# Performance work log

Measured on AMD Instinct MI355X. Metric: run time of the kernel, lower is better.

The kernel has to match this reference:

```python
import jax, jax.numpy as jnp
import numpy as np

MARGIN = 2.0
EPS = 1e-6  # F.pairwise_distance default: norm of (x1 - x2 + eps)

N, D = 4096, 768


def setup_inputs() -> dict:
    key = jax.random.key(0)
    k1, k2, k3 = jax.random.split(key, 3)
    image_embedding = jax.random.normal(k1, (N, D), dtype=jnp.float32)
    text_embedding = jax.random.normal(k2, (N, D), dtype=jnp.float32)
    ground_truth = jax.random.randint(k3, (N, N), 0, 2, dtype=jnp.int32)
    return {
        "image_embedding": image_embedding,
        "text_embedding": text_embedding,
        "ground_truth": ground_truth,
    }


def reference(image_embedding, text_embedding, ground_truth):
    d = image_embedding.shape[1]
    # Pairwise squared distance with pairwise_distance's +eps on the diff:
    # ||a - b + eps||^2 = ||a||^2 + ||b||^2 - 2 a.b + 2 eps (sum a - sum b) + d eps^2
    sa = jnp.sum(image_embedding * image_embedding, axis=1)   # [n]
    sb = jnp.sum(text_embedding * text_embedding, axis=1)     # [n]
    dot = image_embedding @ text_embedding.T                  # [n, n]
    ra = jnp.sum(image_embedding, axis=1)                     # [n]
    rb = jnp.sum(text_embedding, axis=1)                      # [n]
    sq = (sa[:, None] + sb[None, :] - 2.0 * dot
          + 2.0 * EPS * (ra[:, None] - rb[None, :]) + d * EPS * EPS)
    dist = jnp.sqrt(jnp.maximum(sq, 0.0))                     # [n, n]
    label = ground_truth.astype(dist.dtype)
    hinge = jnp.maximum(MARGIN - dist, 0.0)
    loss = jnp.mean((1.0 - label) * dist * dist + label * hinge * hinge)
    return loss
```

## Files before the change

kernel.cpp:

```cpp
#include <hip/hip_runtime.h>
#include <hip/hip_bf16.h>
#include <stdint.h>
#include <stddef.h>


#define NROWS 4096
#define DIM   768
#define BM    128
#define BN    128
#define BK    32
#define MARGIN 2.0f
#define EPSV   1e-6f

typedef __bf16 bf16_t;
typedef bf16_t bf16x8 __attribute__((ext_vector_type(8)));
typedef float  f32x4  __attribute__((ext_vector_type(4)));

__global__ __launch_bounds__(256) void prep_kernel(
    const float* __restrict__ A, const float* __restrict__ B,
    bf16_t* __restrict__ Ab, bf16_t* __restrict__ Bb,
    float* __restrict__ sa, float* __restrict__ sb,
    float* __restrict__ ra, float* __restrict__ rb)
{
    const int row  = blockIdx.x;
    const int isB  = blockIdx.y;
    const float* X = isB ? B : A;
    bf16_t* Xb     = isB ? Bb : Ab;
    float* sdst    = isB ? sb : sa;
    float* rdst    = isB ? rb : ra;

    const int t = threadIdx.x;
    const float* xr = X + (size_t)row * DIM;
    float v0 = xr[t], v1 = xr[t + 256], v2 = xr[t + 512];
    bf16_t* xb = Xb + (size_t)row * DIM;
    xb[t]       = (bf16_t)v0;
    xb[t + 256] = (bf16_t)v1;
    xb[t + 512] = (bf16_t)v2;

    float sum = v0 + v1 + v2;
    float sq  = v0 * v0 + v1 * v1 + v2 * v2;
    #pragma unroll
    for (int off = 32; off > 0; off >>= 1) {
        sum += __shfl_down(sum, off);
        sq  += __shfl_down(sq,  off);
    }
    __shared__ float red[8];
    const int wave = t >> 6;
    if ((t & 63) == 0) { red[wave] = sum; red[4 + wave] = sq; }
    __syncthreads();
    if (t == 0) {
        rdst[row] = (red[0] + red[1]) + (red[2] + red[3]);
        sdst[row] = (red[4] + red[5]) + (red[6] + red[7]);
    }
}

__global__ __launch_bounds__(256) void loss_kernel(
    const bf16_t* __restrict__ A, const bf16_t* __restrict__ B,
    const float* __restrict__ sa, const float* __restrict__ sb,
    const float* __restrict__ ra, const float* __restrict__ rb,
    const int* __restrict__ gt, float* __restrict__ out)
{
    __shared__ __align__(16) bf16_t As[BM * BK];
    __shared__ __align__(16) bf16_t Bs[BN * BK];
    __shared__ float redp[4];

    const int tid  = threadIdx.x;
    const int wave = tid >> 6;
    const int lane = tid & 63;
    const int m0 = blockIdx.y * BM;
    const int n0 = blockIdx.x * BN;

    f32x4 acc[4][4] = {};

    const int lrow   = lane >> 2;
    const int kchunk = (lane & 3) ^ (lrow & 3);

    const int fr = lane & 15;
    const int q  = lane >> 4;
    const int wm = (wave >> 1) * 64;
    const int wn = (wave & 1) * 64;
    const int slot = (q ^ (fr & 3)) * 8;

    for (int k0 = 0; k0 < DIM; k0 += BK) {
        __syncthreads();
        #pragma unroll
        for (int t = 0; t < 2; ++t) {
            const int seg  = wave + 4 * t;
            const int grow = seg * 16 + lrow;
            const bf16_t* ga = A + (size_t)(m0 + grow) * DIM + k0 + kchunk * 8;
            const bf16_t* gb = B + (size_t)(n0 + grow) * DIM + k0 + kchunk * 8;
            __builtin_amdgcn_global_load_lds(
                (const __attribute__((address_space(1))) void*)ga,
                (__attribute__((address_space(3))) void*)(As + seg * 16 * BK),
                16, 0, 0);
            __builtin_amdgcn_global_load_lds(
                (const __attribute__((address_space(1))) void*)gb,
                (__attribute__((address_space(3))) void*)(Bs + seg * 16 * BK),
                16, 0, 0);
        }
        __syncthreads();

        bf16x8 af[4], bfrag[4];
        #pragma unroll
        for (int i = 0; i < 4; ++i) {
            af[i]    = *(const bf16x8*)(As + (wm + i * 16 + fr) * BK + slot);
            bfrag[i] = *(const bf16x8*)(Bs + (wn + i * 16 + fr) * BK + slot);
        }
        #pragma unroll
        for (int mi = 0; mi < 4; ++mi)
            #pragma unroll
            for (int ni = 0; ni < 4; ++ni)
                acc[mi][ni] = __builtin_amdgcn_mfma_f32_16x16x32_bf16(
                    af[mi], bfrag[ni], acc[mi][ni], 0, 0, 0);
    }

    const int cq = lane & 15;
    const int rq = (lane >> 4) * 4;

    float sbv[4], rbv[4];
    #pragma unroll
    for (int ni = 0; ni < 4; ++ni) {
        const int col = n0 + wn + ni * 16 + cq;
        sbv[ni] = sb[col];
        rbv[ni] = rb[col];
    }

    float local = 0.0f;
    #pragma unroll
    for (int mi = 0; mi < 4; ++mi) {
        #pragma unroll
        for (int rr = 0; rr < 4; ++rr) {
            const int row = m0 + wm + mi * 16 + rq + rr;
            const float sav = sa[row];
            const float rav = ra[row];
            const int* gtr = gt + (size_t)row * NROWS + n0 + wn + cq;
            #pragma unroll
            for (int ni = 0; ni < 4; ++ni) {
                const float dot = acc[mi][ni][rr];
                float sqv = sav + sbv[ni] - 2.0f * dot
                          + (2.0f * EPSV) * (rav - rbv[ni])
                          + (float)DIM * EPSV * EPSV;
                float msq  = fmaxf(sqv, 0.0f);
                float dist = sqrtf(msq);
                float h    = fmaxf(MARGIN - dist, 0.0f);
                const int lbl = gtr[ni * 16];
                local += lbl ? (h * h) : msq;
            }
        }
    }

    #pragma unroll
    for (int off = 32; off > 0; off >>= 1) local += __shfl_down(local, off);
    if (lane == 0) redp[wave] = local;
    __syncthreads();
    if (tid == 0) {
        const float s = (redp[0] + redp[1]) + (redp[2] + redp[3]);
        atomicAdd(out, s * (1.0f / (4096.0f * 4096.0f)));
    }
}

extern "C" void kernel_launch(void* const* d_in, const int* in_sizes, int n_in,
                              void* d_out, int out_size, void* d_ws, size_t ws_size,
                              hipStream_t stream)
{
    const float* A  = (const float*)d_in[0];
    const float* B  = (const float*)d_in[1];
    const int*   gt = (const int*)d_in[2];
    float* out = (float*)d_out;

    char* ws = (char*)d_ws;
    const size_t NB = (size_t)NROWS * DIM * sizeof(bf16_t);
    bf16_t* Ab = (bf16_t*)(ws);
    bf16_t* Bb = (bf16_t*)(ws + NB);
    float* sa = (float*)(ws + 2 * NB);
    float* sb = (float*)(ws + 2 * NB + 16384);
    float* ra = (float*)(ws + 2 * NB + 32768);
    float* rb = (float*)(ws + 2 * NB + 49152);

    hipMemsetAsync(d_out, 0, sizeof(float) * (size_t)out_size, stream);
    prep_kernel<<<dim3(NROWS, 2), 256, 0, stream>>>(A, B, Ab, Bb, sa, sb, ra, rb);
    loss_kernel<<<dim3(NROWS / BN, NROWS / BM), 256, 0, stream>>>(
        Ab, Bb, sa, sb, ra, rb, gt, out);
}
```

Baseline: 161.0 us.

## Bit-pack labels, double BK, vectorize prep with one row per wave

Adds a pack kernel that turns the int32 ground-truth matrix into 64-bit ballot masks, so the loss epilogue reads bits instead of scattered int loads. The GEMM K-tile grows from 32 to 64 with an 8-way XOR swizzle and two MFMA sub-steps per barrier pair, halving the number of sync rounds. The prep kernel now handles one row per wave with float4 loads and no shared-memory reduction. It adds a kernel launch, and the 64MB label matrix is still read once in the pack pass, which costs an extra write and read of the packed form.

```diff
diff --git a/kernel.cpp b/kernel.cpp
--- a/kernel.cpp
+++ b/kernel.cpp
@@ -8,12 +8,13 @@
 #define DIM   768
 #define BM    128
 #define BN    128
-#define BK    32
+#define BK    64
 #define MARGIN 2.0f
 #define EPSV   1e-6f
 
 typedef __bf16 bf16_t;
 typedef bf16_t bf16x8 __attribute__((ext_vector_type(8)));
+typedef bf16_t bf16x4 __attribute__((ext_vector_type(4)));
 typedef float  f32x4  __attribute__((ext_vector_type(4)));
 
 __global__ __launch_bounds__(256) void prep_kernel(
@@ -22,43 +23,57 @@
     float* __restrict__ sa, float* __restrict__ sb,
     float* __restrict__ ra, float* __restrict__ rb)
 {
-    const int row  = blockIdx.x;
+    const int tid  = threadIdx.x;
+    const int wave = tid >> 6;
+    const int lane = tid & 63;
+    const int row  = blockIdx.x * 4 + wave;
     const int isB  = blockIdx.y;
     const float* X = isB ? B : A;
     bf16_t* Xb     = isB ? Bb : Ab;
     float* sdst    = isB ? sb : sa;
     float* rdst    = isB ? rb : ra;
 
-    const int t = threadIdx.x;
-    const float* xr = X + (size_t)row * DIM;
-    float v0 = xr[t], v1 = xr[t + 256], v2 = xr[t + 512];
-    bf16_t* xb = Xb + (size_t)row * DIM;
-    xb[t]       = (bf16_t)v0;
-    xb[t + 256] = (bf16_t)v1;
-    xb[t + 512] = (bf16_t)v2;
-
-    float sum = v0 + v1 + v2;
-    float sq  = v0 * v0 + v1 * v1 + v2 * v2;
+    const float4* xr = (const float4*)(X + (size_t)row * DIM);
+    bf16x4* xb = (bf16x4*)(Xb + (size_t)row * DIM);
+
+    float sum = 0.0f, sq = 0.0f;
+    #pragma unroll
+    for (int j = 0; j < 3; ++j) {
+        float4 v = xr[lane + 64 * j];
+        bf16x4 o;
+        o[0] = (bf16_t)v.x; o[1] = (bf16_t)v.y;
+        o[2] = (bf16_t)v.z; o[3] = (bf16_t)v.w;
+        xb[lane + 64 * j] = o;
+        sum += (v.x + v.y) + (v.z + v.w);
+        sq  += v.x * v.x + v.y * v.y + v.z * v.z + v.w * v.w;
+    }
     #pragma unroll
     for (int off = 32; off > 0; off >>= 1) {
         sum += __shfl_down(sum, off);
         sq  += __shfl_down(sq,  off);
     }
-    __shared__ float red[8];
-    const int wave = t >> 6;
-    if ((t & 63) == 0) { red[wave] = sum; red[4 + wave] = sq; }
-    __syncthreads();
-    if (t == 0) {
-        rdst[row] = (red[0] + red[1]) + (red[2] + red[3]);
-        sdst[row] = (red[4] + red[5]) + (red[6] + red[7]);
-    }
-}
-
-__global__ __launch_bounds__(256) void loss_kernel(
+    if (lane == 0) { rdst[row] = sum; sdst[row] = sq; }
+}
+
+__global__ __launch_bounds__(256) void pack_kernel(
+    const int* __restrict__ gt, unsigned long long* __restrict__ gtp)
+{
+    const int lane = threadIdx.x & 63;
+    const int wid  = blockIdx.x * 4 + (threadIdx.x >> 6);
+    const size_t base = (size_t)wid * 128;
+    #pragma unroll 4
+    for (int i = 0; i < 128; ++i) {
+        const int v = gt[(base + i) * 64 + lane];
+        const unsigned long long m = __ballot(v != 0);
+        if (lane == 0) gtp[base + i] = m;
+    }
+}
+
+__global__ __launch_bounds__(256, 4) void loss_kernel(
     const bf16_t* __restrict__ A, const bf16_t* __restrict__ B,
     const float* __restrict__ sa, const float* __restrict__ sb,
     const float* __restrict__ ra, const float* __restrict__ rb,
-    const int* __restrict__ gt, float* __restrict__ out)
+    const uint2* __restrict__ gtp, float* __restrict__ out)
 {
     __shared__ __align__(16) bf16_t As[BM * BK];
     __shared__ __align__(16) bf16_t Bs[BN * BK];
@@ -72,50 +87,55 @@
 
     f32x4 acc[4][4] = {};
 
-    const int lrow   = lane >> 2;
-    const int kchunk = (lane & 3) ^ (lrow & 3);
+    const int lrow = lane >> 3;
+    const int gc   = (lane & 7) ^ lrow;
 
     const int fr = lane & 15;
     const int q  = lane >> 4;
     const int wm = (wave >> 1) * 64;
     const int wn = (wave & 1) * 64;
-    const int slot = (q ^ (fr & 3)) * 8;
 
     for (int k0 = 0; k0 < DIM; k0 += BK) {
         __syncthreads();
         #pragma unroll
-        for (int t = 0; t < 2; ++t) {
-            const int seg  = wave + 4 * t;
-            const int grow = seg * 16 + lrow;
-            const bf16_t* ga = A + (size_t)(m0 + grow) * DIM + k0 + kchunk * 8;
-            const bf16_t* gb = B + (size_t)(n0 + grow) * DIM + k0 + kchunk * 8;
+        for (int s = 0; s < 4; ++s) {
+            const int rowbase = s * 32 + wave * 8;
+            const int grow    = rowbase + lrow;
+            const bf16_t* ga = A + (size_t)(m0 + grow) * DIM + k0 + gc * 8;
+            const bf16_t* gb = B + (size_t)(n0 + grow) * DIM + k0 + gc * 8;
             __builtin_amdgcn_global_load_lds(
                 (const __attribute__((address_space(1))) void*)ga,
-                (__attribute__((address_space(3))) void*)(As + seg * 16 * BK),
+                (__attribute__((address_space(3))) void*)(As + rowbase * BK),
                 16, 0, 0);
             __builtin_amdgcn_global_load_lds(
                 (const __attribute__((address_space(1))) void*)gb,
-                (__attribute__((address_space(3))) void*)(Bs + seg * 16 * BK),
+                (__attribute__((address_space(3))) void*)(Bs + rowbase * BK),
                 16, 0, 0);
         }
         __syncthreads();
 
-        bf16x8 af[4], bfrag[4];
         #pragma unroll
-        for (int i = 0; i < 4; ++i) {
-            af[i]    = *(const bf16x8*)(As + (wm + i * 16 + fr) * BK + slot);
-            bfrag[i] = *(const bf16x8*)(Bs + (wn + i * 16 + fr) * BK + slot);
+        for (int kk = 0; kk < 2; ++kk) {
+            bf16x8 af[4], bfr[4];
+            const int c = kk * 4 + q;
+            #pragma unroll
+            for (int i = 0; i < 4; ++i) {
+                const int pos = (c ^ (fr & 7)) * 8;
+                af[i]  = *(const bf16x8*)(As + (wm + i * 16 + fr) * BK + pos);
+                bfr[i] = *(const bf16x8*)(Bs + (wn + i * 16 + fr) * BK + pos);
+            }
+            #pragma unroll
+            for (int mi = 0; mi < 4; ++mi)
+                #pragma unroll
+                for (int ni = 0; ni < 4; ++ni)
+                    acc[mi][ni] = __builtin_amdgcn_mfma_f32_16x16x32_bf16(
+                        af[mi], bfr[ni], acc[mi][ni], 0, 0, 0);
         }
-        #pragma unroll
-        for (int mi = 0; mi < 4; ++mi)
-            #pragma unroll
-            for (int ni = 0; ni < 4; ++ni)
-                acc[mi][ni] = __builtin_amdgcn_mfma_f32_16x16x32_bf16(
-                    af[mi], bfrag[ni], acc[mi][ni], 0, 0, 0);
     }
 
     const int cq = lane & 15;
     const int rq = (lane >> 4) * 4;
+    const int cb = (n0 + wn) >> 6;
 
     float sbv[4], rbv[4];
     #pragma unroll
@@ -133,7 +153,7 @@
             const int row = m0 + wm + mi * 16 + rq + rr;
             const float sav = sa[row];
             const float rav = ra[row];
-            const int* gtr = gt + (size_t)row * NROWS + n0 + wn + cq;
+            const uint2 w = gtp[(size_t)row * (NROWS / 64) + cb];
             #pragma unroll
             for (int ni = 0; ni < 4; ++ni) {
                 const float dot = acc[mi][ni][rr];
@@ -143,8 +163,9 @@
                 float msq  = fmaxf(sqv, 0.0f);
                 float dist = sqrtf(msq);
                 float h    = fmaxf(MARGIN - dist, 0.0f);
-                const int lbl = gtr[ni * 16];
-                local += lbl ? (h * h) : msq;
+                const unsigned wd = (ni < 2) ? w.x : w.y;
+                const unsigned g  = (wd >> (cq + (ni & 1) * 16)) & 1u;
+                local += g ? (h * h) : msq;
             }
         }
     }
@@ -176,9 +197,11 @@
     float* sb = (float*)(ws + 2 * NB + 16384);
     float* ra = (float*)(ws + 2 * NB + 32768);
     float* rb = (float*)(ws + 2 * NB + 49152);
+    unsigned long long* gtp = (unsigned long long*)(ws + 2 * NB + 65536);
 
     hipMemsetAsync(d_out, 0, sizeof(float) * (size_t)out_size, stream);
-    prep_kernel<<<dim3(NROWS, 2), 256, 0, stream>>>(A, B, Ab, Bb, sa, sb, ra, rb);
+    prep_kernel<<<dim3(NROWS / 4, 2), 256, 0, stream>>>(A, B, Ab, Bb, sa, sb, ra, rb);
+    pack_kernel<<<dim3(512), 256, 0, stream>>>(gt, gtp);
     loss_kernel<<<dim3(NROWS / BN, NROWS / BM), 256, 0, stream>>>(
-        Ab, Bb, sa, sb, ra, rb, gt, out);
-}
+        Ab, Bb, sa, sb, ra, rb, (const uint2*)gtp, out);
+}
```

After: 205.1 us. +27.3%, slower.
